# Kernel optimization log

Measured on AMD Instinct MI355X. Metric: run time of the kernel, lower is better.

Reference implementation:

```python
import jax, jax.numpy as jnp
import numpy as np

B = 65536  # number of 32-bit words processed by the VM


def _build_tables():
    # ByteToNibbleFFN: byte one-hot -> (high, low) nibble one-hots
    W1_b2n = np.eye(256, dtype=np.float32)
    W2_b2n = np.zeros((256, 32), dtype=np.float32)
    for b in range(256):
        W2_b2n[b, (b >> 4) & 15] = 1.0
        W2_b2n[b, 16 + (b & 15)] = 1.0
    # NibbleToByteFFN: (high, low) -> byte one-hot
    W1_n2b = np.zeros((32, 256), dtype=np.float32)
    for high in range(16):
        for low in range(16):
            bv = (high << 4) | low
            W1_n2b[high, bv] = 1.0
            W1_n2b[16 + low, bv] = 1.0
    W2_n2b = np.eye(256, dtype=np.float32)
    # NibbleTableFFN for XOR
    W1_xor = np.zeros((32, 256), dtype=np.float32)
    W2_xor = np.zeros((256, 16), dtype=np.float32)
    for a in range(16):
        for b in range(16):
            k = a * 16 + b
            W1_xor[a, k] = 1.0
            W1_xor[16 + b, k] = 1.0
            W2_xor[k, (a ^ b) & 15] = 1.0
    # NibbleAddFFN: (a, b, carry) -> (sum, carry)
    W1_add = np.zeros((34, 512), dtype=np.float32)
    W2_sum = np.zeros((512, 16), dtype=np.float32)
    W2_carry = np.zeros((512, 2), dtype=np.float32)
    for a in range(16):
        for b in range(16):
            for c in range(2):
                k = a * 32 + b * 2 + c
                W1_add[a, k] = 1.0
                W1_add[16 + b, k] = 1.0
                W1_add[32 + c, k] = 1.0
                total = a + b + c
                W2_sum[k, total & 15] = 1.0
                W2_carry[k, 1 if total >= 16 else 0] = 1.0
    return (jnp.asarray(W1_b2n), jnp.asarray(W2_b2n), jnp.asarray(W1_n2b),
            jnp.asarray(W2_n2b), jnp.asarray(W1_xor), jnp.asarray(W2_xor),
            jnp.asarray(W1_add), jnp.asarray(W2_sum), jnp.asarray(W2_carry))


def setup_inputs() -> dict:
    key = jax.random.key(0)
    k1, k2 = jax.random.split(key)
    a_idx = jax.random.randint(k1, (B, 4), 0, 256)
    b_idx = jax.random.randint(k2, (B, 4), 0, 256)
    a_bytes = jax.nn.one_hot(a_idx, 256, dtype=jnp.float32)  # [B,4,256]
    b_bytes = jax.nn.one_hot(b_idx, 256, dtype=jnp.float32)
    (W1_b2n, W2_b2n, W1_n2b, W2_n2b, W1_xor, W2_xor,
     W1_add, W2_sum, W2_carry) = _build_tables()
    return {
        'a_bytes': a_bytes, 'b_bytes': b_bytes,
        'W1_b2n': W1_b2n, 'W2_b2n': W2_b2n,
        'W1_n2b': W1_n2b, 'W2_n2b': W2_n2b,
        'W1_xor': W1_xor, 'W2_xor': W2_xor,
        'W1_add': W1_add, 'W2_sum': W2_sum, 'W2_carry': W2_carry,
    }


def reference(a_bytes, b_bytes, W1_b2n, W2_b2n, W1_n2b, W2_n2b,
              W1_xor, W2_xor, W1_add, W2_sum, W2_carry):
    # Batched faithful translation of the torch VM: the torch code loops over
    # single words; here each op is vectorized over the word batch B while the
    # fixed 4-byte carry chain remains an explicit (structural) loop.
    def byte_to_nib(x):                       # x: [B,256]
        w = jax.nn.softmax((x @ W1_b2n) * 100.0, axis=-1)
        nib = w @ W2_b2n                      # [B,32]
        return nib[:, :16], nib[:, 16:]

    def nib_to_byte(high, low):               # [B,16] each -> [B,256]
        x = jnp.concatenate([high, low], axis=-1)
        w = jax.nn.softmax((x @ W1_n2b - 1.5) * 20.0, axis=-1)
        return w @ W2_n2b

    def nib_xor(a, b):                        # [B,16] each -> [B,16]
        x = jnp.concatenate([a, b], axis=-1)
        w = jax.nn.softmax((x @ W1_xor - 1.5) * 20.0, axis=-1)
        return w @ W2_xor

    def nib_add(a, b, c):                     # [B,16],[B,16],[B,2]
        x = jnp.concatenate([a, b, c], axis=-1)
        w = jax.nn.softmax((x @ W1_add - 2.5) * 20.0, axis=-1)
        return w @ W2_sum, w @ W2_carry

    def byte_xor(a, b):                       # [B,256] each
        a_h, a_l = byte_to_nib(a)
        b_h, b_l = byte_to_nib(b)
        return nib_to_byte(nib_xor(a_h, b_h), nib_xor(a_l, b_l))

    n = a_bytes.shape[0]
    # ByteAddFFN: 4-byte ripple-carry add, carry starts as one-hot 0
    carry = jnp.broadcast_to(jnp.array([1.0, 0.0], dtype=a_bytes.dtype), (n, 2))
    sum_bytes = []
    for i in range(4):
        a_h, a_l = byte_to_nib(a_bytes[:, i])
        b_h, b_l = byte_to_nib(b_bytes[:, i])
        r_low, carry_low = nib_add(a_l, b_l, carry)
        r_high, carry = nib_add(a_h, b_h, carry_low)
        sum_bytes.append(nib_to_byte(r_high, r_low))
    # Chain a second VM op: XOR the sum with operand a, per byte
    out = [byte_xor(sum_bytes[i], a_bytes[:, i]) for i in range(4)]
    return jnp.stack(out, axis=1)             # [B,4,256]
```

## Files before the change

kernel.cpp:

```cpp
#include <hip/hip_runtime.h>
#include <stdint.h>

__global__ __launch_bounds__(256) void vm_kernel(
    const float* __restrict__ a_bytes,
    const float* __restrict__ b_bytes,
    float* __restrict__ out)
{
    const int word     = blockIdx.x;
    const int t        = threadIdx.x;
    const int byte_pos = t >> 6;
    const int lane     = t & 63;
    const long base = (long)word * 1024 + byte_pos * 256 + lane * 4;

    const float4 av = *(const float4*)(a_bytes + base);
    const float4 bv = *(const float4*)(b_bytes + base);

    const float j0 = (float)(lane * 4);
    float pa = av.x * j0 + av.y * (j0 + 1.0f) + av.z * (j0 + 2.0f) + av.w * (j0 + 3.0f);
    float pb = bv.x * j0 + bv.y * (j0 + 1.0f) + bv.z * (j0 + 2.0f) + bv.w * (j0 + 3.0f);
#pragma unroll
    for (int off = 32; off >= 1; off >>= 1) {
        pa += __shfl_xor(pa, off, 64);
        pb += __shfl_xor(pb, off, 64);
    }

    __shared__ int a_idx[4];
    __shared__ int b_idx[4];
    __shared__ int out_idx[4];
    if (lane == 0) {
        a_idx[byte_pos] = (int)(pa + 0.5f);
        b_idx[byte_pos] = (int)(pb + 0.5f);
    }
    __syncthreads();
    if (t == 0) {
        uint32_t aw = (uint32_t)a_idx[0] | ((uint32_t)a_idx[1] << 8) |
                      ((uint32_t)a_idx[2] << 16) | ((uint32_t)a_idx[3] << 24);
        uint32_t bw = (uint32_t)b_idx[0] | ((uint32_t)b_idx[1] << 8) |
                      ((uint32_t)b_idx[2] << 16) | ((uint32_t)b_idx[3] << 24);
        uint32_t s = aw + bw;
        uint32_t o = s ^ aw;
        out_idx[0] = (int)(o & 255u);
        out_idx[1] = (int)((o >> 8) & 255u);
        out_idx[2] = (int)((o >> 16) & 255u);
        out_idx[3] = (int)((o >> 24) & 255u);
    }
    __syncthreads();

    const int oi = out_idx[byte_pos];
    const int j  = lane * 4;
    float4 ov;
    ov.x = (j     == oi) ? 1.0f : 0.0f;
    ov.y = (j + 1 == oi) ? 1.0f : 0.0f;
    ov.z = (j + 2 == oi) ? 1.0f : 0.0f;
    ov.w = (j + 3 == oi) ? 1.0f : 0.0f;
    *(float4*)(out + base) = ov;
}

extern "C" void kernel_launch(void* const* d_in, const int* in_sizes, int n_in,
                              void* d_out, int out_size, void* d_ws, size_t ws_size,
                              hipStream_t stream)
{
    const float* a_bytes = (const float*)d_in[0];
    const float* b_bytes = (const float*)d_in[1];
    float* out = (float*)d_out;
    const int n_words = in_sizes[0] / 1024;
    vm_kernel<<<n_words, 256, 0, stream>>>(a_bytes, b_bytes, out);
}
```

Baseline: 578.5 us.

## Map one wavefront per word and decode one-hot indices with ballots

Each 64-lane wavefront now handles a full 4-byte word, loading all four 256-float rows per lane and finding the hot index with wave ballots instead of a weighted shuffle reduction. This removes shared memory, both block barriers and the single-thread serial section. It also puts more independent loads in flight per thread. It relies on inputs being exact one-hot rows, which the float-sum decode also assumed.

```diff
diff --git a/kernel.cpp b/kernel.cpp
--- a/kernel.cpp
+++ b/kernel.cpp
@@ -1,68 +1,67 @@
 #include <hip/hip_runtime.h>
 #include <stdint.h>
 
+
+__device__ __forceinline__ uint32_t row_index(float4 v) {
+    const bool nx = v.x != 0.0f, ny = v.y != 0.0f, nz = v.z != 0.0f, nw = v.w != 0.0f;
+    const unsigned long long m  = __ballot(nx | ny | nz | nw);
+    const unsigned long long m0 = __ballot(ny | nw);
+    const unsigned long long m1 = __ballot(nz | nw);
+    const int src = __ffsll(m) - 1;
+    return ((uint32_t)src << 2) |
+           (uint32_t)((m0 >> src) & 1ull) |
+           ((uint32_t)((m1 >> src) & 1ull) << 1);
+}
+
+__device__ __forceinline__ float4 onehot4(int j, uint32_t oi) {
+    float4 r;
+    r.x = ((uint32_t)j     == oi) ? 1.0f : 0.0f;
+    r.y = ((uint32_t)j + 1 == oi) ? 1.0f : 0.0f;
+    r.z = ((uint32_t)j + 2 == oi) ? 1.0f : 0.0f;
+    r.w = ((uint32_t)j + 3 == oi) ? 1.0f : 0.0f;
+    return r;
+}
+
 __global__ __launch_bounds__(256) void vm_kernel(
-    const float* __restrict__ a_bytes,
-    const float* __restrict__ b_bytes,
-    float* __restrict__ out)
+    const float4* __restrict__ a4,
+    const float4* __restrict__ b4,
+    float4* __restrict__ o4,
+    int n_words)
 {
-    const int word     = blockIdx.x;
-    const int t        = threadIdx.x;
-    const int byte_pos = t >> 6;
-    const int lane     = t & 63;
-    const long base = (long)word * 1024 + byte_pos * 256 + lane * 4;
+    const int word = (blockIdx.x << 2) | (threadIdx.x >> 6);
+    const int lane = threadIdx.x & 63;
+    if (word >= n_words) return;
 
-    const float4 av = *(const float4*)(a_bytes + base);
-    const float4 bv = *(const float4*)(b_bytes + base);
+    const long base = (long)word * 256 + lane;
 
-    const float j0 = (float)(lane * 4);
-    float pa = av.x * j0 + av.y * (j0 + 1.0f) + av.z * (j0 + 2.0f) + av.w * (j0 + 3.0f);
-    float pb = bv.x * j0 + bv.y * (j0 + 1.0f) + bv.z * (j0 + 2.0f) + bv.w * (j0 + 3.0f);
-#pragma unroll
-    for (int off = 32; off >= 1; off >>= 1) {
-        pa += __shfl_xor(pa, off, 64);
-        pb += __shfl_xor(pb, off, 64);
-    }
+    const float4 av0 = a4[base];       const float4 av1 = a4[base + 64];
+    const float4 av2 = a4[base + 128]; const float4 av3 = a4[base + 192];
+    const float4 bv0 = b4[base];       const float4 bv1 = b4[base + 64];
+    const float4 bv2 = b4[base + 128]; const float4 bv3 = b4[base + 192];
 
-    __shared__ int a_idx[4];
-    __shared__ int b_idx[4];
-    __shared__ int out_idx[4];
-    if (lane == 0) {
-        a_idx[byte_pos] = (int)(pa + 0.5f);
-        b_idx[byte_pos] = (int)(pb + 0.5f);
-    }
-    __syncthreads();
-    if (t == 0) {
-        uint32_t aw = (uint32_t)a_idx[0] | ((uint32_t)a_idx[1] << 8) |
-                      ((uint32_t)a_idx[2] << 16) | ((uint32_t)a_idx[3] << 24);
-        uint32_t bw = (uint32_t)b_idx[0] | ((uint32_t)b_idx[1] << 8) |
-                      ((uint32_t)b_idx[2] << 16) | ((uint32_t)b_idx[3] << 24);
-        uint32_t s = aw + bw;
-        uint32_t o = s ^ aw;
-        out_idx[0] = (int)(o & 255u);
-        out_idx[1] = (int)((o >> 8) & 255u);
-        out_idx[2] = (int)((o >> 16) & 255u);
-        out_idx[3] = (int)((o >> 24) & 255u);
-    }
-    __syncthreads();
+    const uint32_t aw = row_index(av0)        | (row_index(av1) << 8) |
+                        (row_index(av2) << 16) | (row_index(av3) << 24);
+    const uint32_t bw = row_index(bv0)        | (row_index(bv1) << 8) |
+                        (row_index(bv2) << 16) | (row_index(bv3) << 24);
 
-    const int oi = out_idx[byte_pos];
-    const int j  = lane * 4;
-    float4 ov;
-    ov.x = (j     == oi) ? 1.0f : 0.0f;
-    ov.y = (j + 1 == oi) ? 1.0f : 0.0f;
-    ov.z = (j + 2 == oi) ? 1.0f : 0.0f;
-    ov.w = (j + 3 == oi) ? 1.0f : 0.0f;
-    *(float4*)(out + base) = ov;
+    const uint32_t s = aw + bw;
+    const uint32_t o = s ^ aw;
+
+    const int j = lane * 4;
+    o4[base]       = onehot4(j,  o        & 255u);
+    o4[base + 64]  = onehot4(j, (o >> 8)  & 255u);
+    o4[base + 128] = onehot4(j, (o >> 16) & 255u);
+    o4[base + 192] = onehot4(j, (o >> 24) & 255u);
 }
 
 extern "C" void kernel_launch(void* const* d_in, const int* in_sizes, int n_in,
                               void* d_out, int out_size, void* d_ws, size_t ws_size,
                               hipStream_t stream)
 {
-    const float* a_bytes = (const float*)d_in[0];
-    const float* b_bytes = (const float*)d_in[1];
-    float* out = (float*)d_out;
+    const float4* a4 = (const float4*)d_in[0];
+    const float4* b4 = (const float4*)d_in[1];
+    float4* o4 = (float4*)d_out;
     const int n_words = in_sizes[0] / 1024;
-    vm_kernel<<<n_words, 256, 0, stream>>>(a_bytes, b_bytes, out);
+    const int n_blocks = (n_words + 3) / 4;
+    vm_kernel<<<n_blocks, 256, 0, stream>>>(a4, b4, o4, n_words);
 }
```

Measured after the change: 593.2 us. 1.03x slower.
